# Kernel tuning notes

Hardware: AMD Instinct MI355X
Metric: run time of the kernel (lower is better)

The kernel has to match this reference:

```python
import jax, jax.numpy as jnp
import numpy as np

LN_EPS = 1e-6  # flax LayerNorm default


def setup_inputs() -> dict:
    B, S, D, H, HD = 4, 2048, 1024, 16, 64
    key = jax.random.key(0)
    ks = jax.random.split(key, 3)
    x = jax.random.normal(ks[0], (B, S, D), dtype=jnp.float32)
    mask = jnp.tril(jnp.ones((S, S), dtype=bool))[None, None]  # causal [1,1,S,S]
    ln_scale = jnp.ones((D,), jnp.float32)
    ln_bias = jnp.zeros((D,), jnp.float32)
    w_qkv = jax.random.normal(ks[1], (D, H, 3 * HD), jnp.float32) * (1.0 / np.sqrt(D))
    b_qkv = jnp.zeros((H, 3 * HD), jnp.float32)
    w_out = jax.random.normal(ks[2], (D, D), jnp.float32) * (1.0 / np.sqrt(D))
    b_out = jnp.zeros((D,), jnp.float32)
    return {"x": x, "mask": mask, "ln_scale": ln_scale, "ln_bias": ln_bias,
            "w_qkv": w_qkv, "b_qkv": b_qkv, "w_out": w_out, "b_out": b_out}


def _layernorm(x, scale, bias):
    mu = jnp.mean(x, axis=-1, keepdims=True)
    var = jnp.var(x, axis=-1, keepdims=True)
    return (x - mu) * jax.lax.rsqrt(var + LN_EPS) * scale + bias


def reference(x, mask, ln_scale, ln_bias, w_qkv, b_qkv, w_out, b_out):
    B, S, D = x.shape
    xn = _layernorm(x, ln_scale, ln_bias)                      # [B,S,D]
    qkv = jnp.einsum('bsd,dhf->bshf', xn, w_qkv) + b_qkv        # [B,S,H,3*hd]
    q, k, v = jnp.split(qkv, 3, axis=-1)                        # each [B,S,H,hd]
    scale = q.shape[-1] ** (-0.5)
    q = q * scale
    q = q.transpose(0, 2, 1, 3)                                 # [B,H,S,hd]
    k = k.transpose(0, 2, 1, 3)
    v = v.transpose(0, 2, 1, 3)
    attn = q @ k.swapaxes(-2, -1)                               # [B,H,S,S]
    attn = jnp.where(mask, attn, jnp.finfo(jnp.float32).min)
    attn = jax.nn.softmax(attn, axis=-1)
    y = attn @ v                                                # [B,H,S,hd]
    y = y.transpose(0, 2, 1, 3).reshape(B, S, D)
    y = y @ w_out + b_out                                       # [B,S,D]
    return y
```

## Files before the change

### kernel.cpp

```cpp
#include <hip/hip_runtime.h>

typedef unsigned short u16;
typedef unsigned int u32;
typedef __bf16 bf16x8 __attribute__((ext_vector_type(8)));
typedef float f32x4 __attribute__((ext_vector_type(4)));
typedef u16 u16x8 __attribute__((ext_vector_type(8)));
typedef u16 u16x4 __attribute__((ext_vector_type(4)));

#define GLOBAL_AS __attribute__((address_space(1)))
#define LDS_AS __attribute__((address_space(3)))

#define LOG2E 1.4426950408889634f
#define SMAX_C2 34.62468097703102f

__device__ __forceinline__ void async16(const u16* g, u16* l) {
  __builtin_amdgcn_global_load_lds((const GLOBAL_AS void*)g, (LDS_AS void*)l, 16, 0, 0);
}

__device__ __forceinline__ float bf2f(u16 u) {
  union { unsigned int i; float f; } v; v.i = ((unsigned int)u) << 16; return v.f;
}
__device__ __forceinline__ u16 f2bf(float f) {
  __bf16 h = (__bf16)f;
  return __builtin_bit_cast(u16, h);
}

__device__ __forceinline__ int swz(int r, int c) {
  return r * 64 + (c ^ ((r & 7) << 3));
}

__global__ __launch_bounds__(256) void prep_k(const float* __restrict__ x,
                                              const float* __restrict__ gamma,
                                              const float* __restrict__ beta,
                                              u16* __restrict__ xn,
                                              const float* __restrict__ wq,
                                              u16* __restrict__ wTq,
                                              const float* __restrict__ wo,
                                              u16* __restrict__ wTo) {
  __shared__ u16 tile[32][33];
  __shared__ float red[8];
  int id = blockIdx.x;
  if (id < 8192) {
    const int t = threadIdx.x, wid = t >> 6, lane = t & 63;
    const float* xr = x + (size_t)id * 1024;
    float4 v = *(const float4*)&xr[t * 4];
    float s = v.x + v.y + v.z + v.w;
    float ss = v.x * v.x + v.y * v.y + v.z * v.z + v.w * v.w;
    #pragma unroll
    for (int off = 32; off >= 1; off >>= 1) {
      s += __shfl_xor(s, off, 64);
      ss += __shfl_xor(ss, off, 64);
    }
    if (lane == 0) { red[wid] = s; red[4 + wid] = ss; }
    __syncthreads();
    s = red[0] + red[1] + red[2] + red[3];
    ss = red[4] + red[5] + red[6] + red[7];
    const float mu = s * (1.0f / 1024.0f);
    const float var = ss * (1.0f / 1024.0f) - mu * mu;
    const float rstd = rsqrtf(var + 1e-6f);
    float4 gv = *(const float4*)&gamma[t * 4];
    float4 bv = *(const float4*)&beta[t * 4];
    ushort4 o;
    o.x = f2bf((v.x - mu) * rstd * gv.x + bv.x);
    o.y = f2bf((v.y - mu) * rstd * gv.y + bv.y);
    o.z = f2bf((v.z - mu) * rstd * gv.z + bv.z);
    o.w = f2bf((v.w - mu) * rstd * gv.w + bv.w);
    *(ushort4*)&xn[(size_t)id * 1024 + t * 4] = o;
    return;
  }
  id -= 8192;
  const float* in; u16* out; int R, C, bx, by;
  if (id < 3072) { in = wq; out = wTq; R = 1024; C = 3072; bx = id % 96; by = id / 96; }
  else { id -= 3072; in = wo; out = wTo; R = 1024; C = 1024; bx = id & 31; by = id >> 5; }
  const int c0 = bx * 32, r0 = by * 32;
  const int tx = threadIdx.x & 31, ty = threadIdx.x >> 5;
  #pragma unroll
  for (int i = 0; i < 32; i += 8)
    tile[ty + i][tx] = f2bf(in[(size_t)(r0 + ty + i) * C + c0 + tx]);
  __syncthreads();
  #pragma unroll
  for (int i = 0; i < 32; i += 8)
    out[(size_t)(c0 + ty + i) * R + r0 + tx] = tile[tx][ty + i];
}

template <typename OutT>
__global__ __launch_bounds__(256) void gemm_bt(const u16* __restrict__ A,
                                               const u16* __restrict__ Bt,
                                               const float* __restrict__ bias,
                                               OutT* __restrict__ C,
                                               int M, int N, int K) {
  __shared__ __align__(16) u16 As[3][128 * 32];
  __shared__ __align__(16) u16 Bs[3][128 * 32];
  const int tid = threadIdx.x, wid = tid >> 6, lane = tid & 63;
  const int row = lane & 15, q4 = lane >> 4;
  const int m0 = blockIdx.y * 128, n0 = blockIdx.x * 128;
  const int wm = (wid >> 1) * 64, wn = (wid & 1) * 64;
  f32x4 acc[4][4] = {};
  const int sr = wid * 16 + (lane >> 2);
  const int sk = (lane & 3) * 8;
  const u16* gA0 = A + (size_t)(m0 + sr) * K + sk;
  const u16* gA1 = A + (size_t)(m0 + 64 + sr) * K + sk;
  const u16* gB0 = Bt + (size_t)(n0 + sr) * K + sk;
  const u16* gB1 = Bt + (size_t)(n0 + 64 + sr) * K + sk;
  const int lw = wid * 512;
  const int NT = K >> 5;

  async16(gA0, &As[0][lw]);
  async16(gA1, &As[0][2048 + lw]);
  async16(gB0, &Bs[0][lw]);
  async16(gB1, &Bs[0][2048 + lw]);
  async16(gA0 + 32, &As[1][lw]);
  async16(gA1 + 32, &As[1][2048 + lw]);
  async16(gB0 + 32, &Bs[1][lw]);
  async16(gB1 + 32, &Bs[1][2048 + lw]);

  int bc = 0, bs = 2;
  for (int kt = 0; kt < NT; ++kt) {
    asm volatile("s_waitcnt vmcnt(4)" ::: "memory");
    __builtin_amdgcn_s_barrier();
    __builtin_amdgcn_sched_barrier(0);
    if (kt + 2 < NT) {
      const int k0 = (kt + 2) << 5;
      async16(gA0 + k0, &As[bs][lw]);
      async16(gA1 + k0, &As[bs][2048 + lw]);
      async16(gB0 + k0, &Bs[bs][lw]);
      async16(gB1 + k0, &Bs[bs][2048 + lw]);
    }
    __builtin_amdgcn_sched_barrier(0);
    bf16x8 af[4], bfv[4];
    #pragma unroll
    for (int mt = 0; mt < 4; ++mt)
      af[mt] = *(const bf16x8*)&As[bc][(wm + mt * 16 + row) * 32 + q4 * 8];
    #pragma unroll
    for (int nt = 0; nt < 4; ++nt)
      bfv[nt] = *(const bf16x8*)&Bs[bc][(wn + nt * 16 + row) * 32 + q4 * 8];
    #pragma unroll
    for (int mt = 0; mt < 4; ++mt)
      #pragma unroll
      for (int nt = 0; nt < 4; ++nt)
        acc[mt][nt] = __builtin_amdgcn_mfma_f32_16x16x32_bf16(
            af[mt], bfv[nt], acc[mt][nt], 0, 0, 0);
    bs = bc;
    bc = (bc + 1 == 3) ? 0 : bc + 1;
  }
  #pragma unroll
  for (int nt = 0; nt < 4; ++nt) {
    const int gn = n0 + wn + nt * 16 + row;
    const float bv = bias[gn];
    #pragma unroll
    for (int mt = 0; mt < 4; ++mt) {
      const int gm = m0 + wm + mt * 16 + q4 * 4;
      #pragma unroll
      for (int r = 0; r < 4; ++r) {
        const float val = acc[mt][nt][r] + bv;
        if constexpr (sizeof(OutT) == 2)
          C[(size_t)(gm + r) * N + gn] = (OutT)f2bf(val);
        else
          C[(size_t)(gm + r) * N + gn] = (OutT)val;
      }
    }
  }
}

__global__ __launch_bounds__(256, 3) void attn_k(const u16* __restrict__ qkv,
                                                 u16* __restrict__ y) {
  __shared__ __align__(16) u16 Ks[2][64 * 64];
  __shared__ __align__(16) u16 Vs[2][64 * 64];
  __shared__ __align__(16) u16 Ps[4][2][16 * 64];
  const int tid = threadIdx.x, wid = tid >> 6, lane = tid & 63;
  const int row = lane & 15, q4 = lane >> 4;
  const int id = blockIdx.x;
  const int qb = 15 - (id >> 6);
  const int h = (id & 63) >> 2, b = id & 3;
  const size_t seq0 = (size_t)b * 2048;
  const u16* base = qkv + seq0 * 3072 + h * 192;
  const int kk = tid >> 2, ko = tid & 3;
  const int kp = tid & 31, dg = tid >> 5;

  bf16x8 ones;
  #pragma unroll
  for (int j = 0; j < 8; ++j) ones[j] = (__bf16)1.0f;

  const int rgmin = qb * 128 + wid * 32;
  const int rgmax = rgmin + 31;
  bf16x8 qf[2][2];
  #pragma unroll
  for (int g = 0; g < 2; ++g) {
    const u16* qp = base + (size_t)(rgmin + g * 16 + row) * 3072;
    qf[g][0] = *(const bf16x8*)(qp + q4 * 8);
    qf[g][1] = *(const bf16x8*)(qp + 32 + q4 * 8);
    #pragma unroll
    for (int j = 0; j < 8; ++j) {
      qf[g][0][j] = (__bf16)((float)qf[g][0][j] * 0.125f);
      qf[g][1][j] = (__bf16)((float)qf[g][1][j] * 0.125f);
    }
  }
  f32x4 l4[2] = {};
  f32x4 o[2][4] = {};
  const int ktiles = 2 * qb + 2;

  const u16* kg = base + (size_t)kk * 3072 + 64 + ko * 8;
  const u16* vg = base + (size_t)(2 * kp) * 3072 + 128 + dg * 8;
  u16x8 kr0 = *(const u16x8*)kg;
  u16x8 kr1 = *(const u16x8*)(kg + 32);
  u16x8 va = *(const u16x8*)vg;
  u16x8 vb = *(const u16x8*)(vg + 3072);
  *(u16x8*)&Ks[0][swz(kk, ko * 8)] = kr0;
  *(u16x8*)&Ks[0][swz(kk, ko * 8 + 32)] = kr1;
  #pragma unroll
  for (int j = 0; j < 8; ++j)
    *(u32*)&Vs[0][swz(dg * 8 + j, 2 * kp)] = (u32)va[j] | ((u32)vb[j] << 16);
  if (ktiles > 1) {
    kr0 = *(const u16x8*)(kg + (size_t)64 * 3072);
    kr1 = *(const u16x8*)(kg + (size_t)64 * 3072 + 32);
    va = *(const u16x8*)(vg + (size_t)64 * 3072);
    vb = *(const u16x8*)(vg + (size_t)65 * 3072);
  }
  __syncthreads();

  for (int kt = 0; kt < ktiles; ++kt) {
    const int kbase = kt * 64;
    const int cur = kt & 1;
    if (kt + 1 < ktiles) {
      *(u16x8*)&Ks[cur ^ 1][swz(kk, ko * 8)] = kr0;
      *(u16x8*)&Ks[cur ^ 1][swz(kk, ko * 8 + 32)] = kr1;
      #pragma unroll
      for (int j = 0; j < 8; ++j)
        *(u32*)&Vs[cur ^ 1][swz(dg * 8 + j, 2 * kp)] =
            (u32)va[j] | ((u32)vb[j] << 16);
      if (kt + 2 < ktiles) {
        const size_t nb = (size_t)(kbase + 128) * 3072;
        kr0 = *(const u16x8*)(kg + nb);
        kr1 = *(const u16x8*)(kg + nb + 32);
        va = *(const u16x8*)(vg + nb);
        vb = *(const u16x8*)(vg + nb + 3072);
      }
    }

    if (kbase <= rgmax) {
      #pragma unroll
      for (int nt = 0; nt < 4; ++nt) {
        bf16x8 kf0 = *(const bf16x8*)&Ks[cur][swz(nt * 16 + row, q4 * 8)];
        bf16x8 kf1 = *(const bf16x8*)&Ks[cur][swz(nt * 16 + row, 32 + q4 * 8)];
        #pragma unroll
        for (int g = 0; g < 2; ++g) {
          f32x4 z = {0.f, 0.f, 0.f, 0.f};
          z = __builtin_amdgcn_mfma_f32_16x16x32_bf16(qf[g][0], kf0, z, 0, 0, 0);
          z = __builtin_amdgcn_mfma_f32_16x16x32_bf16(qf[g][1], kf1, z, 0, 0, 0);
          const int rb = rgmin + g * 16;
          const bool mn = (kbase + 63 > rb);
          const int d = kbase + nt * 16 + row - rb - q4 * 4;
          u16* pw = Ps[wid][g];
          #pragma unroll
          for (int r = 0; r < 4; ++r) {
            const float bias = (mn && d > r) ? -1e30f : -SMAX_C2;
            const float p = __builtin_amdgcn_exp2f(fmaf(z[r], LOG2E, bias));
            pw[swz(q4 * 4 + r, nt * 16 + row)] = f2bf(p);
          }
        }
      }

      bf16x8 pf[2][2];
      #pragma unroll
      for (int g = 0; g < 2; ++g) {
        pf[g][0] = *(const bf16x8*)&Ps[wid][g][swz(row, q4 * 8)];
        pf[g][1] = *(const bf16x8*)&Ps[wid][g][swz(row, 32 + q4 * 8)];
        l4[g] = __builtin_amdgcn_mfma_f32_16x16x32_bf16(pf[g][0], ones, l4[g], 0, 0, 0);
        l4[g] = __builtin_amdgcn_mfma_f32_16x16x32_bf16(pf[g][1], ones, l4[g], 0, 0, 0);
      }

      #pragma unroll
      for (int t = 0; t < 4; ++t) {
        bf16x8 vf0 = *(const bf16x8*)&Vs[cur][swz(t * 16 + row, q4 * 8)];
        bf16x8 vf1 = *(const bf16x8*)&Vs[cur][swz(t * 16 + row, 32 + q4 * 8)];
        #pragma unroll
        for (int g = 0; g < 2; ++g) {
          o[g][t] = __builtin_amdgcn_mfma_f32_16x16x32_bf16(pf[g][0], vf0, o[g][t], 0, 0, 0);
          o[g][t] = __builtin_amdgcn_mfma_f32_16x16x32_bf16(pf[g][1], vf1, o[g][t], 0, 0, 0);
        }
      }
    }
    __syncthreads();
  }

  #pragma unroll
  for (int g = 0; g < 2; ++g) {
    const int srow = rgmin + g * 16 + q4 * 4;
    float inv[4];
    #pragma unroll
    for (int r = 0; r < 4; ++r) inv[r] = 1.0f / l4[g][r];
    #pragma unroll
    for (int t = 0; t < 4; ++t)
      #pragma unroll
      for (int r = 0; r < 4; ++r)
        y[(seq0 + srow + r) * 1024 + h * 64 + t * 16 + row] =
            f2bf(o[g][t][r] * inv[r]);
  }
}

extern "C" void kernel_launch(void* const* d_in, const int* in_sizes, int n_in,
                              void* d_out, int out_size, void* d_ws, size_t ws_size,
                              hipStream_t stream) {
  const float* x     = (const float*)d_in[0];
  const float* ln_s  = (const float*)d_in[2];
  const float* ln_b  = (const float*)d_in[3];
  const float* w_qkv = (const float*)d_in[4];
  const float* b_qkv = (const float*)d_in[5];
  const float* w_out = (const float*)d_in[6];
  const float* b_out = (const float*)d_in[7];
  float* out = (float*)d_out;

  u16* qkv   = (u16*)d_ws;
  u16* xn    = qkv + (size_t)8192 * 3072;
  u16* wTq   = xn + (size_t)8192 * 1024;
  u16* wTo   = wTq + (size_t)3072 * 1024;
  u16* yattn = xn;

  prep_k<<<12288, 256, 0, stream>>>(x, ln_s, ln_b, xn, w_qkv, wTq, w_out, wTo);
  gemm_bt<u16><<<dim3(24, 64), 256, 0, stream>>>(xn, wTq, b_qkv, qkv, 8192, 3072, 1024);
  attn_k<<<1024, 256, 0, stream>>>(qkv, yattn);
  gemm_bt<float><<<dim3(8, 64), 256, 0, stream>>>(yattn, wTo, b_out, out, 8192, 1024, 1024);
}
```

Baseline: 259.5 us.

## Load GEMM B operand directly to registers and swizzle A tile in LDS

The bf16 GEMM stops staging the B tile through LDS. Each wave now loads its B fragments straight from global memory into double-buffered registers, while A keeps its three-stage async LDS pipeline with an XOR swizzle to cut bank conflicts. The k-loop is unrolled by two to alternate the register buffers, the vmcnt waits are adjusted to match, and launch bounds request two blocks per SM. This halves LDS use and LDS traffic, but B is read redundantly by waves that share columns, and the kernel may stall on global latency for the register prefetch.

Measured after the change: 319.8 us. +23.2%, slower.

```diff
diff --git a/kernel.cpp b/kernel.cpp
--- a/kernel.cpp
+++ b/kernel.cpp
@@ -84,65 +84,88 @@
 }
 
 template <typename OutT>
-__global__ __launch_bounds__(256) void gemm_bt(const u16* __restrict__ A,
-                                               const u16* __restrict__ Bt,
-                                               const float* __restrict__ bias,
-                                               OutT* __restrict__ C,
-                                               int M, int N, int K) {
-  __shared__ __align__(16) u16 As[3][128 * 32];
-  __shared__ __align__(16) u16 Bs[3][128 * 32];
+__global__ __launch_bounds__(256, 2) void gemm_bt(const u16* __restrict__ A,
+                                                  const u16* __restrict__ Bt,
+                                                  const float* __restrict__ bias,
+                                                  OutT* __restrict__ C,
+                                                  int M, int N, int K) {
+  __shared__ __align__(16) u16 As[3][4096];
   const int tid = threadIdx.x, wid = tid >> 6, lane = tid & 63;
   const int row = lane & 15, q4 = lane >> 4;
   const int m0 = blockIdx.y * 128, n0 = blockIdx.x * 128;
   const int wm = (wid >> 1) * 64, wn = (wid & 1) * 64;
   f32x4 acc[4][4] = {};
   const int sr = wid * 16 + (lane >> 2);
-  const int sk = (lane & 3) * 8;
+  const int sk = (((lane & 3) ^ ((lane >> 3) & 3))) * 8;
+  const int xr = ((lane & 15) >> 1) & 3;
   const u16* gA0 = A + (size_t)(m0 + sr) * K + sk;
   const u16* gA1 = A + (size_t)(m0 + 64 + sr) * K + sk;
-  const u16* gB0 = Bt + (size_t)(n0 + sr) * K + sk;
-  const u16* gB1 = Bt + (size_t)(n0 + 64 + sr) * K + sk;
+  const u16* pB[4];
+  #pragma unroll
+  for (int nt = 0; nt < 4; ++nt)
+    pB[nt] = Bt + (size_t)(n0 + wn + nt * 16 + row) * K + q4 * 8;
   const int lw = wid * 512;
   const int NT = K >> 5;
 
   async16(gA0, &As[0][lw]);
   async16(gA1, &As[0][2048 + lw]);
-  async16(gB0, &Bs[0][lw]);
-  async16(gB1, &Bs[0][2048 + lw]);
   async16(gA0 + 32, &As[1][lw]);
   async16(gA1 + 32, &As[1][2048 + lw]);
-  async16(gB0 + 32, &Bs[1][lw]);
-  async16(gB1 + 32, &Bs[1][2048 + lw]);
+  __builtin_amdgcn_sched_barrier(0);
+  bf16x8 b0[4], b1[4];
+  #pragma unroll
+  for (int nt = 0; nt < 4; ++nt) b0[nt] = *(const bf16x8*)(pB[nt]);
+  __builtin_amdgcn_sched_barrier(0);
+  #pragma unroll
+  for (int nt = 0; nt < 4; ++nt) b1[nt] = *(const bf16x8*)(pB[nt] + 32);
+  __builtin_amdgcn_sched_barrier(0);
 
   int bc = 0, bs = 2;
-  for (int kt = 0; kt < NT; ++kt) {
-    asm volatile("s_waitcnt vmcnt(4)" ::: "memory");
-    __builtin_amdgcn_s_barrier();
-    __builtin_amdgcn_sched_barrier(0);
-    if (kt + 2 < NT) {
-      const int k0 = (kt + 2) << 5;
-      async16(gA0 + k0, &As[bs][lw]);
-      async16(gA1 + k0, &As[bs][2048 + lw]);
-      async16(gB0 + k0, &Bs[bs][lw]);
-      async16(gB1 + k0, &Bs[bs][2048 + lw]);
-    }
-    __builtin_amdgcn_sched_barrier(0);
-    bf16x8 af[4], bfv[4];
-    #pragma unroll
-    for (int mt = 0; mt < 4; ++mt)
-      af[mt] = *(const bf16x8*)&As[bc][(wm + mt * 16 + row) * 32 + q4 * 8];
-    #pragma unroll
-    for (int nt = 0; nt < 4; ++nt)
-      bfv[nt] = *(const bf16x8*)&Bs[bc][(wn + nt * 16 + row) * 32 + q4 * 8];
-    #pragma unroll
-    for (int mt = 0; mt < 4; ++mt)
-      #pragma unroll
-      for (int nt = 0; nt < 4; ++nt)
-        acc[mt][nt] = __builtin_amdgcn_mfma_f32_16x16x32_bf16(
-            af[mt], bfv[nt], acc[mt][nt], 0, 0, 0);
-    bs = bc;
-    bc = (bc + 1 == 3) ? 0 : bc + 1;
-  }
+#define GEMM_STEP(KT, BCUR, BNEXT)                                           \
+  {                                                                          \
+    const int kt = (KT);                                                     \
+    if (kt == 0)                                                             \
+      asm volatile("s_waitcnt vmcnt(4)" ::: "memory");                       \
+    else if (kt + 1 < NT)                                                    \
+      asm volatile("s_waitcnt vmcnt(2)" ::: "memory");                       \
+    else                                                                     \
+      asm volatile("s_waitcnt vmcnt(0)" ::: "memory");                       \
+    __builtin_amdgcn_s_barrier();                                            \
+    __builtin_amdgcn_sched_barrier(0);                                       \
+    if (kt > 0 && kt + 1 < NT) {    \
+      const int koff = (kt + 1) << 5;                                        \
+      _Pragma("unroll")                                                      \
+      for (int nt = 0; nt < 4; ++nt)                                         \
+        BNEXT[nt] = *(const bf16x8*)(pB[nt] + koff);                         \
+    }                                                                        \
+    __builtin_amdgcn_sched_barrier(0);                                       \
+    if (kt + 2 < NT) {                                                       \
+      const int k0 = (kt + 2) << 5;                                          \
+      async16(gA0 + k0, &As[bs][lw]);                                        \
+      async16(gA1 + k0, &As[bs][2048 + lw]);                                 \
+    }                                                                        \
+    __builtin_amdgcn_sched_barrier(0);                                       \
+    bf16x8 af[4];                                                            \
+    _Pragma("unroll")                                                        \
+    for (int mt = 0; mt < 4; ++mt)                                           \
+      af[mt] = *(const bf16x8*)&As[bc][(wm + mt * 16 + row) * 32 +           \
+                                       ((q4 ^ xr) * 8)];                     \
+    _Pragma("unroll")                                                        \
+    for (int mt = 0; mt < 4; ++mt)                                           \
+      _Pragma("unroll")                                                      \
+      for (int nt = 0; nt < 4; ++nt)                                         \
+        acc[mt][nt] = __builtin_amdgcn_mfma_f32_16x16x32_bf16(               \
+            af[mt], BCUR[nt], acc[mt][nt], 0, 0, 0);                         \
+    bs = bc;                                                                 \
+    bc = (bc + 1 == 3) ? 0 : bc + 1;                                         \
+  }
+
+  for (int kt2 = 0; kt2 < NT; kt2 += 2) {
+    GEMM_STEP(kt2, b0, b1);
+    GEMM_STEP(kt2 + 1, b1, b0);
+  }
+#undef GEMM_STEP
+
   #pragma unroll
   for (int nt = 0; nt < 4; ++nt) {
     const int gn = n0 + wn + nt * 16 + row;
```
